# Performance work log

Measured on AMD Instinct MI355X. Metric: run time of the kernel, lower is better.

Reference implementation:

```python
import jax, jax.numpy as jnp
import numpy as np

B, S, F, DK = 4, 2048, 1024, 1024

def setup_inputs() -> dict:
    key = jax.random.key(0)
    ks = jax.random.split(key, 9)
    sF = 1.0 / np.sqrt(F)
    sD = 1.0 / np.sqrt(DK)
    return {
        "x":  jax.random.normal(ks[0], (B, S, F), dtype=jnp.float32),
        "Wq": jax.random.normal(ks[1], (DK, F), dtype=jnp.float32) * sF,
        "bq": jax.random.normal(ks[2], (DK,), dtype=jnp.float32) * sF,
        "Wk": jax.random.normal(ks[3], (DK, F), dtype=jnp.float32) * sF,
        "bk": jax.random.normal(ks[4], (DK,), dtype=jnp.float32) * sF,
        "Wv": jax.random.normal(ks[5], (DK, F), dtype=jnp.float32) * sF,
        "bv": jax.random.normal(ks[6], (DK,), dtype=jnp.float32) * sF,
        "Wo": jax.random.normal(ks[7], (F, DK), dtype=jnp.float32) * sD,
        "bo": jax.random.normal(ks[8], (F,), dtype=jnp.float32) * sD,
    }

def reference(x, Wq, bq, Wk, bk, Wv, bv, Wo, bo):
    # Linear layers (torch convention: y = x @ W.T + b)
    q = jnp.einsum('bsf,df->bsd', x, Wq) + bq  # (B,S,DK)
    k = jnp.einsum('bsf,df->bsd', x, Wk) + bk  # (B,S,DK)
    v = jnp.einsum('bsf,df->bsd', x, Wv) + bv  # (B,S,DK)
    scale = 1.0 / (q.shape[-1] ** 0.5)
    scores = jnp.einsum('bqd,bkd->bqk', q, k) * scale  # (B,Sq,Sk)
    # Faithful to original: softmax over dim=-2 (the QUERY axis)
    attn = jax.nn.softmax(scores, axis=-2)
    ctx = jnp.einsum('bqk,bkd->bqd', attn, v)  # (B,S,DK)
    out = jnp.einsum('bsd,fd->bsf', ctx, Wo) + bo  # (B,S,F)
    return out
```

## Files before the change

### kernel.cpp

```cpp
#include <hip/hip_runtime.h>
#include <hip/hip_bf16.h>
#include <math.h>

typedef __bf16 bf16_t;
typedef __bf16 bf16x8 __attribute__((ext_vector_type(8)));
typedef float f32x4 __attribute__((ext_vector_type(4)));


__device__ __forceinline__ void g2l16(const bf16_t* g, bf16_t* l) {
  __builtin_amdgcn_global_load_lds(
      (const __attribute__((address_space(1))) void*)g,
      (__attribute__((address_space(3))) void*)l, 16, 0, 0);
}

__device__ __forceinline__ float waveSum(float v) {
#pragma unroll
  for (int o = 32; o > 0; o >>= 1) v += __shfl_xor(v, o);
  return v;
}

__device__ __forceinline__ void xcdswz(int& bx, int& by, int& bz) {
  const int gx = gridDim.x, gy = gridDim.y;
  const int n = gx * gy * gridDim.z;
  int f = bx + gx * (by + gy * bz);
  const int cpx = n >> 3;
  int s = (f & 7) * cpx + (f >> 3);
  bx = s % gx; s /= gx; by = s % gy; bz = s / gy;
}

__device__ __forceinline__ bf16x8 rdf(const char* base, int row, int kbyte) {
  int off = (row << 7) + kbyte;
  off ^= (row & 7) << 4;
  return *reinterpret_cast<const bf16x8*>(base + off);
}


__global__ __launch_bounds__(256) void cast_f32_to_bf16(
    const float* __restrict__ in, bf16_t* __restrict__ out, long n) {
  long i = ((long)blockIdx.x * 256 + threadIdx.x) * 8;
  if (i >= n) return;
  float4 a = *reinterpret_cast<const float4*>(in + i);
  float4 b = *reinterpret_cast<const float4*>(in + i + 4);
  bf16x8 o;
  o[0] = (bf16_t)a.x; o[1] = (bf16_t)a.y; o[2] = (bf16_t)a.z; o[3] = (bf16_t)a.w;
  o[4] = (bf16_t)b.x; o[5] = (bf16_t)b.y; o[6] = (bf16_t)b.z; o[7] = (bf16_t)b.w;
  *reinterpret_cast<bf16x8*>(out + i) = o;
}

__global__ __launch_bounds__(256) void cast_w4(
    const float* __restrict__ w0, const float* __restrict__ w1,
    const float* __restrict__ w2, const float* __restrict__ w3,
    bf16_t* __restrict__ o0, bf16_t* __restrict__ o1,
    bf16_t* __restrict__ o2, bf16_t* __restrict__ o3) {
  const int sel = blockIdx.x >> 9;
  const int blk = blockIdx.x & 511;
  const float* in = sel == 0 ? w0 : (sel == 1 ? w1 : (sel == 2 ? w2 : w3));
  bf16_t* out = sel == 0 ? o0 : (sel == 1 ? o1 : (sel == 2 ? o2 : o3));
  long i = ((long)blk * 256 + threadIdx.x) * 8;
  float4 a = *reinterpret_cast<const float4*>(in + i);
  float4 b = *reinterpret_cast<const float4*>(in + i + 4);
  bf16x8 o;
  o[0] = (bf16_t)a.x; o[1] = (bf16_t)a.y; o[2] = (bf16_t)a.z; o[3] = (bf16_t)a.w;
  o[4] = (bf16_t)b.x; o[5] = (bf16_t)b.y; o[6] = (bf16_t)b.z; o[7] = (bf16_t)b.w;
  *reinterpret_cast<bf16x8*>(out + i) = o;
}


#define STAGE256(d, o, h, t) do {                                              \
  const bf16_t* gsrc_ = ((o) ? Bb : Ab) + (long)((h) * 128 + srl) * K +        \
                        (long)(t) * 64 + sgsw;                                 \
  bf16_t* ldsb_ = &lds[d][o][(h) * 8192] + ldst;                               \
  g2l16(gsrc_, ldsb_);                                                         \
  g2l16(gsrc_ + 64L * K, ldsb_ + 4096);                                        \
} while (0)

#define AREAD256(d, qm) do {                                                   \
  const char* Ab_ = (const char*)&lds[d][0][0];                                \
  int r_ = (qm) * 128 + wr2 * 64 + rA;                                         \
  a0 = rdf(Ab_, r_, kb);      a1 = rdf(Ab_, r_, kb + 64);                      \
  a2 = rdf(Ab_, r_ + 16, kb); a3 = rdf(Ab_, r_ + 16, kb + 64);                 \
  a4 = rdf(Ab_, r_ + 32, kb); a5 = rdf(Ab_, r_ + 32, kb + 64);                 \
  a6 = rdf(Ab_, r_ + 48, kb); a7 = rdf(Ab_, r_ + 48, kb + 64);                 \
} while (0)

#define BREAD256(d, qn, r0v, r1v, r2v, r3v) do {                               \
  const char* Bb_ = (const char*)&lds[d][1][0];                                \
  int c_ = (qn) * 128 + wc2 * 32 + rA;                                         \
  r0v = rdf(Bb_, c_, kb);      r1v = rdf(Bb_, c_, kb + 64);                    \
  r2v = rdf(Bb_, c_ + 16, kb); r3v = rdf(Bb_, c_ + 16, kb + 64);               \
} while (0)

#define MFMA16(qm, qn, b0v, b1v, b2v, b3v) do {                                \
  acc[(qm)*4+0][(qn)*2+0] = __builtin_amdgcn_mfma_f32_16x16x32_bf16(a0, b0v, acc[(qm)*4+0][(qn)*2+0], 0,0,0); \
  acc[(qm)*4+0][(qn)*2+0] = __builtin_amdgcn_mfma_f32_16x16x32_bf16(a1, b1v, acc[(qm)*4+0][(qn)*2+0], 0,0,0); \
  acc[(qm)*4+1][(qn)*2+0] = __builtin_amdgcn_mfma_f32_16x16x32_bf16(a2, b0v, acc[(qm)*4+1][(qn)*2+0], 0,0,0); \
  acc[(qm)*4+1][(qn)*2+0] = __builtin_amdgcn_mfma_f32_16x16x32_bf16(a3, b1v, acc[(qm)*4+1][(qn)*2+0], 0,0,0); \
  acc[(qm)*4+2][(qn)*2+0] = __builtin_amdgcn_mfma_f32_16x16x32_bf16(a4, b0v, acc[(qm)*4+2][(qn)*2+0], 0,0,0); \
  acc[(qm)*4+2][(qn)*2+0] = __builtin_amdgcn_mfma_f32_16x16x32_bf16(a5, b1v, acc[(qm)*4+2][(qn)*2+0], 0,0,0); \
  acc[(qm)*4+3][(qn)*2+0] = __builtin_amdgcn_mfma_f32_16x16x32_bf16(a6, b0v, acc[(qm)*4+3][(qn)*2+0], 0,0,0); \
  acc[(qm)*4+3][(qn)*2+0] = __builtin_amdgcn_mfma_f32_16x16x32_bf16(a7, b1v, acc[(qm)*4+3][(qn)*2+0], 0,0,0); \
  acc[(qm)*4+0][(qn)*2+1] = __builtin_amdgcn_mfma_f32_16x16x32_bf16(a0, b2v, acc[(qm)*4+0][(qn)*2+1], 0,0,0); \
  acc[(qm)*4+0][(qn)*2+1] = __builtin_amdgcn_mfma_f32_16x16x32_bf16(a1, b3v, acc[(qm)*4+0][(qn)*2+1], 0,0,0); \
  acc[(qm)*4+1][(qn)*2+1] = __builtin_amdgcn_mfma_f32_16x16x32_bf16(a2, b2v, acc[(qm)*4+1][(qn)*2+1], 0,0,0); \
  acc[(qm)*4+1][(qn)*2+1] = __builtin_amdgcn_mfma_f32_16x16x32_bf16(a3, b3v, acc[(qm)*4+1][(qn)*2+1], 0,0,0); \
  acc[(qm)*4+2][(qn)*2+1] = __builtin_amdgcn_mfma_f32_16x16x32_bf16(a4, b2v, acc[(qm)*4+2][(qn)*2+1], 0,0,0); \
  acc[(qm)*4+2][(qn)*2+1] = __builtin_amdgcn_mfma_f32_16x16x32_bf16(a5, b3v, acc[(qm)*4+2][(qn)*2+1], 0,0,0); \
  acc[(qm)*4+3][(qn)*2+1] = __builtin_amdgcn_mfma_f32_16x16x32_bf16(a6, b2v, acc[(qm)*4+3][(qn)*2+1], 0,0,0); \
  acc[(qm)*4+3][(qn)*2+1] = __builtin_amdgcn_mfma_f32_16x16x32_bf16(a7, b3v, acc[(qm)*4+3][(qn)*2+1], 0,0,0); \
} while (0)

#define VMC(n) asm volatile("s_waitcnt vmcnt(" #n ")" ::: "memory")

#define PH_ENTER() do {                                                        \
  __builtin_amdgcn_s_barrier();                                                \
  asm volatile("s_waitcnt lgkmcnt(0)" ::: "memory");                           \
  __builtin_amdgcn_s_setprio(1);                                               \
} while (0)

#define PH_EXIT() do {                                                         \
  __builtin_amdgcn_s_setprio(0);                                               \
  __builtin_amdgcn_s_barrier();                                                \
} while (0)

template <int EPI>
__launch_bounds__(512, 2)
__global__ void gemm256(const bf16_t* __restrict__ A, const bf16_t* __restrict__ B,
                        int K, float alpha,
                        void* __restrict__ C0, void* __restrict__ C1, void* __restrict__ C2,
                        const float* __restrict__ bias0, const float* __restrict__ bias1,
                        const float* __restrict__ bias2,
                        int Ncols, long sA, long sB, long sC) {
  __shared__ bf16_t lds[2][2][16384];

  int bx = blockIdx.x, by = blockIdx.y, bz = blockIdx.z;
  xcdswz(bx, by, bz);

  const int tid = threadIdx.x;
  const int lane = tid & 63;
  const int w = tid >> 6;
  const int wr2 = w >> 2;
  const int wc2 = w & 3;
  const int rA = lane & 15;
  const int kb = (lane >> 4) << 4;

  const int bm = bx * 256;
  const int bn = by * 256;
  const bf16_t* Ab = A + (long)bz * sA + (long)bm * K;
  const bf16_t* Bb = B + (long)bz * sB + (long)bn * K;

  const int srl = tid >> 3;
  const int sgr = tid & 7;
  const int sgsw = (sgr ^ (srl & 7)) * 8;
  const int ldst = srl * 64 + sgr * 8;

  f32x4 acc[8][4] = {};
  bf16x8 a0, a1, a2, a3, a4, a5, a6, a7;
  bf16x8 p0, p1, p2, p3, q0, q1, q2, q3;

  const int NT = K >> 6;

  STAGE256(0, 0, 0, 0);
  STAGE256(0, 1, 0, 0);
  STAGE256(0, 1, 1, 0);
  STAGE256(0, 0, 1, 0);
  STAGE256(1, 0, 0, 1);
  STAGE256(1, 1, 0, 1);
  STAGE256(1, 1, 1, 1);
  STAGE256(1, 0, 1, 1);
  VMC(12);
  __builtin_amdgcn_s_barrier();

  int t = 0;
  for (int it = 0; it < NT / 2 - 1; ++it, t += 2) {
    AREAD256(0, 0); BREAD256(0, 0, p0, p1, p2, p3);
    VMC(10);
    PH_ENTER(); MFMA16(0, 0, p0, p1, p2, p3); PH_EXIT();
    BREAD256(0, 1, q0, q1, q2, q3);
    STAGE256(0, 0, 0, t + 2); STAGE256(0, 1, 0, t + 2);
    VMC(12);
    PH_ENTER(); MFMA16(0, 1, q0, q1, q2, q3); PH_EXIT();
    AREAD256(0, 1);
    STAGE256(0, 1, 1, t + 2);
    PH_ENTER(); MFMA16(1, 0, p0, p1, p2, p3); PH_EXIT();
    STAGE256(0, 0, 1, t + 2);
    VMC(12);
    PH_ENTER(); MFMA16(1, 1, q0, q1, q2, q3); PH_EXIT();
    AREAD256(1, 0); BREAD256(1, 0, p0, p1, p2, p3);
    VMC(10);
    PH_ENTER(); MFMA16(0, 0, p0, p1, p2, p3); PH_EXIT();
    BREAD256(1, 1, q0, q1, q2, q3);
    STAGE256(1, 0, 0, t + 3); STAGE256(1, 1, 0, t + 3);
    VMC(12);
    PH_ENTER(); MFMA16(0, 1, q0, q1, q2, q3); PH_EXIT();
    AREAD256(1, 1);
    STAGE256(1, 1, 1, t + 3);
    PH_ENTER(); MFMA16(1, 0, p0, p1, p2, p3); PH_EXIT();
    STAGE256(1, 0, 1, t + 3);
    VMC(12);
    PH_ENTER(); MFMA16(1, 1, q0, q1, q2, q3); PH_EXIT();
  }

  AREAD256(0, 0); BREAD256(0, 0, p0, p1, p2, p3);
  VMC(10);
  PH_ENTER(); MFMA16(0, 0, p0, p1, p2, p3); PH_EXIT();
  BREAD256(0, 1, q0, q1, q2, q3);
  VMC(8);
  PH_ENTER(); MFMA16(0, 1, q0, q1, q2, q3); PH_EXIT();
  AREAD256(0, 1);
  PH_ENTER(); MFMA16(1, 0, p0, p1, p2, p3); PH_EXIT();
  VMC(4);
  PH_ENTER(); MFMA16(1, 1, q0, q1, q2, q3); PH_EXIT();
  AREAD256(1, 0); BREAD256(1, 0, p0, p1, p2, p3);
  VMC(2);
  PH_ENTER(); MFMA16(0, 0, p0, p1, p2, p3); PH_EXIT();
  BREAD256(1, 1, q0, q1, q2, q3);
  VMC(0);
  PH_ENTER(); MFMA16(0, 1, q0, q1, q2, q3); PH_EXIT();
  AREAD256(1, 1);
  PH_ENTER(); MFMA16(1, 0, p0, p1, p2, p3); PH_EXIT();
  PH_ENTER(); MFMA16(1, 1, q0, q1, q2, q3); PH_EXIT();

  const int rr = (lane >> 4) * 4;
  const int cc = lane & 15;
#pragma unroll
  for (int qm = 0; qm < 2; ++qm)
#pragma unroll
    for (int m = 0; m < 4; ++m) {
      const int grow = bm + qm * 128 + wr2 * 64 + m * 16 + rr;
#pragma unroll
      for (int qn = 0; qn < 2; ++qn)
#pragma unroll
        for (int n = 0; n < 2; ++n) {
          const int gcol = bn + qn * 128 + wc2 * 32 + n * 16 + cc;
          const f32x4 v = acc[qm * 4 + m][qn * 2 + n];
          if (EPI == 1) {
            const int sel = gcol >> 10;
            const int lcol = gcol & 1023;
            const float* bp = sel == 0 ? bias0 : (sel == 1 ? bias1 : bias2);
            bf16_t* op = sel == 0 ? (bf16_t*)C0 : (sel == 1 ? (bf16_t*)C1 : (bf16_t*)C2);
            const float bv = bp[lcol];
#pragma unroll
            for (int j = 0; j < 4; ++j)
              op[(long)(grow + j) * 1024 + lcol] = (bf16_t)(v[j] + bv);
          } else {
            bf16_t* C = (bf16_t*)C0 + (long)bz * sC;
#pragma unroll
            for (int j = 0; j < 4; ++j)
              C[(long)(grow + j) * Ncols + gcol] = (bf16_t)__expf(v[j] * alpha);
          }
        }
    }
  (void)Ncols;
}


template <int OUT_BF16, int HAS_BIAS>
__launch_bounds__(256, 2)
__global__ void gemm_bt(const bf16_t* __restrict__ A, const bf16_t* __restrict__ B,
                        const float* __restrict__ bias, void* __restrict__ Cv,
                        int M, int N, int K, float alpha,
                        long sA, long sB, long sC) {
  int bxi = blockIdx.x, byi = blockIdx.y, bzi = blockIdx.z;
  xcdswz(bxi, byi, bzi);
  const bf16_t* Ab = A + (long)bzi * sA;
  const bf16_t* Bb = B + (long)bzi * sB;
  const int bm = bxi * 128;
  const int bn = byi * 128;

  __shared__ bf16_t sAt[128 * 32];
  __shared__ bf16_t sBt[128 * 32];

  const int tid = threadIdx.x;
  const int lane = tid & 63;
  const int w = tid >> 6;
  const int wr = (w >> 1) * 64;
  const int wc = (w & 1) * 64;

  f32x4 acc[4][4] = {};

  const int r0 = tid >> 2;
  const int c0 = (tid & 3) * 8;
  const int r1 = 64 + (tid >> 2);
  const long lds0 = (long)tid * 8;
  const long lds1 = 2048 + (long)tid * 8;

  const int arow = wr + (lane & 15);
  const int brow = wc + (lane & 15);
  const int koff = (lane >> 4) * 8;

  const int nK = K >> 5;
  for (int kt = 0; kt < nK; ++kt) {
    const int k0 = kt << 5;
    g2l16(Ab + (long)(bm + r0) * K + k0 + c0, sAt + lds0);
    g2l16(Ab + (long)(bm + r1) * K + k0 + c0, sAt + lds1);
    g2l16(Bb + (long)(bn + r0) * K + k0 + c0, sBt + lds0);
    g2l16(Bb + (long)(bn + r1) * K + k0 + c0, sBt + lds1);
    __syncthreads();

    bf16x8 af[4], bfr[4];
#pragma unroll
    for (int m = 0; m < 4; ++m)
      af[m] = *reinterpret_cast<const bf16x8*>(sAt + (arow + m * 16) * 32 + koff);
#pragma unroll
    for (int n = 0; n < 4; ++n)
      bfr[n] = *reinterpret_cast<const bf16x8*>(sBt + (brow + n * 16) * 32 + koff);
#pragma unroll
    for (int m = 0; m < 4; ++m)
#pragma unroll
      for (int n = 0; n < 4; ++n)
        acc[m][n] = __builtin_amdgcn_mfma_f32_16x16x32_bf16(af[m], bfr[n], acc[m][n], 0, 0, 0);
    __syncthreads();
  }

  const int rbase = bm + wr + (lane >> 4) * 4;
  const int cbase = bn + wc + (lane & 15);
#pragma unroll
  for (int n = 0; n < 4; ++n) {
    const int col = cbase + n * 16;
    float bv = 0.f;
    if (HAS_BIAS) bv = bias[col];
#pragma unroll
    for (int m = 0; m < 4; ++m) {
      const int row0 = rbase + m * 16;
#pragma unroll
      for (int j = 0; j < 4; ++j) {
        float v = acc[m][n][j] * alpha + bv;
        if (OUT_BF16) {
          bf16_t* C = (bf16_t*)Cv + (long)bzi * sC;
          C[(long)(row0 + j) * N + col] = (bf16_t)v;
        } else {
          float* C = (float*)Cv + (long)bzi * sC;
          C[(long)(row0 + j) * N + col] = v;
        }
      }
    }
  }
}


__global__ __launch_bounds__(256) void row_sums(const bf16_t* __restrict__ P,
                                                float* __restrict__ rinv) {
  const long row = blockIdx.x;
  const bf16_t* p = P + row * 2048;
  const int t = threadIdx.x;
  bf16x8 a = *reinterpret_cast<const bf16x8*>(p + t * 8);
  float s = 0.f;
#pragma unroll
  for (int u = 0; u < 8; ++u) s += (float)a[u];
  s = waveSum(s);
  __shared__ float red[4];
  if ((t & 63) == 0) red[t >> 6] = s;
  __syncthreads();
  s = red[0] + red[1] + red[2] + red[3];
  if (t == 0) rinv[row] = 1.0f / s;
}


__global__ __launch_bounds__(256) void scale_T(const bf16_t* __restrict__ P,
                                               const float* __restrict__ rinv,
                                               bf16_t* __restrict__ attn) {
  const int b = blockIdx.z;
  const int q0 = blockIdx.x * 64;
  const int kk0 = blockIdx.y * 64;
  __shared__ bf16_t tile[64][72];
  const int t = threadIdx.x;
  const int i = t >> 2;
  const int qj = (t & 3) * 16;
  const long grow = (long)b * 2048 + kk0 + i;
  const float ri = rinv[grow];
  const bf16_t* src = P + grow * 2048 + q0 + qj;
  bf16x8 v0 = *reinterpret_cast<const bf16x8*>(src);
  bf16x8 v1 = *reinterpret_cast<const bf16x8*>(src + 8);
#pragma unroll
  for (int u = 0; u < 8; ++u) {
    tile[i][qj + u] = (bf16_t)((float)v0[u] * ri);
    tile[i][qj + 8 + u] = (bf16_t)((float)v1[u] * ri);
  }
  __syncthreads();
  const int j = t >> 2;
  const int kc = (t & 3) * 16;
  bf16x8 o0, o1;
#pragma unroll
  for (int u = 0; u < 8; ++u) o0[u] = tile[kc + u][j];
#pragma unroll
  for (int u = 0; u < 8; ++u) o1[u] = tile[kc + 8 + u][j];
  bf16_t* dst = attn + ((long)b * 2048 + q0 + j) * 2048 + kk0 + kc;
  *reinterpret_cast<bf16x8*>(dst) = o0;
  *reinterpret_cast<bf16x8*>(dst + 8) = o1;
}


__global__ __launch_bounds__(256) void transpose_bf16k(const bf16_t* __restrict__ in,
                                                       bf16_t* __restrict__ out,
                                                       int R, int C) {
  const int b = blockIdx.z;
  const int r0 = blockIdx.x * 64;
  const int c0 = blockIdx.y * 64;
  __shared__ bf16_t tile[64][72];
  const int t = threadIdx.x;
  const int i = t >> 2;
  const int cj = (t & 3) * 16;
  const bf16_t* src = in + ((long)b * R + r0 + i) * C + c0 + cj;
  bf16x8 a0 = *reinterpret_cast<const bf16x8*>(src);
  bf16x8 a1 = *reinterpret_cast<const bf16x8*>(src + 8);
#pragma unroll
  for (int u = 0; u < 8; ++u) { tile[i][cj + u] = a0[u]; tile[i][cj + 8 + u] = a1[u]; }
  __syncthreads();
  const int j = t >> 2;
  const int rc = (t & 3) * 16;
  bf16x8 o0, o1;
#pragma unroll
  for (int u = 0; u < 8; ++u) o0[u] = tile[rc + u][j];
#pragma unroll
  for (int u = 0; u < 8; ++u) o1[u] = tile[rc + 8 + u][j];
  bf16_t* dst = out + ((long)b * C + c0 + j) * R + r0 + rc;
  *reinterpret_cast<bf16x8*>(dst) = o0;
  *reinterpret_cast<bf16x8*>(dst + 8) = o1;
}


extern "C" void kernel_launch(void* const* d_in, const int* in_sizes, int n_in,
                              void* d_out, int out_size, void* d_ws, size_t ws_size,
                              hipStream_t stream) {
  const float* x  = (const float*)d_in[0];
  const float* Wq = (const float*)d_in[1];
  const float* bq = (const float*)d_in[2];
  const float* Wk = (const float*)d_in[3];
  const float* bk = (const float*)d_in[4];
  const float* Wv = (const float*)d_in[5];
  const float* bv = (const float*)d_in[6];
  const float* Wo = (const float*)d_in[7];
  const float* bo = (const float*)d_in[8];
  float* out = (float*)d_out;
  char* ws = (char*)d_ws;

  const long MB = 1024L * 1024L;
  bf16_t* xb    = (bf16_t*)(ws + 0);
  bf16_t* Wqkvb = (bf16_t*)(ws + 16 * MB);
  bf16_t* Wob   = (bf16_t*)(ws + 22 * MB);
  bf16_t* Qb    = (bf16_t*)(ws + 24 * MB);
  bf16_t* Kb    = (bf16_t*)(ws + 40 * MB);
  bf16_t* Vb    = (bf16_t*)(ws + 56 * MB);
  bf16_t* Pp    = (bf16_t*)(ws + 72 * MB);
  bf16_t* attn  = (bf16_t*)(ws + 136 * MB);
  float*  rinv  = (float*)(ws + 168 * MB);
  bf16_t* VT    = (bf16_t*)(ws + 0);
  bf16_t* ctxb  = (bf16_t*)(ws + 24 * MB);

  cast_f32_to_bf16<<<4096, 256, 0, stream>>>(x, xb, 8388608);
  cast_w4<<<2048, 256, 0, stream>>>(Wq, Wk, Wv, Wo,
                                    Wqkvb, Wqkvb + 1048576, Wqkvb + 2097152, Wob);

  gemm256<1><<<dim3(32, 12, 1), 512, 0, stream>>>(
      xb, Wqkvb, 1024, 1.0f, Qb, Kb, Vb, bq, bk, bv, 3072, 0, 0, 0);

  gemm256<2><<<dim3(8, 8, 4), 512, 0, stream>>>(
      Kb, Qb, 1024, 0.03125f, Pp, nullptr, nullptr, nullptr, nullptr, nullptr,
      2048, 2048L * 1024, 2048L * 1024, 2048L * 2048);

  row_sums<<<8192, 256, 0, stream>>>(Pp, rinv);
  dim3 gsm(32, 32, 4);
  scale_T<<<gsm, 256, 0, stream>>>(Pp, rinv, attn);

  dim3 gtr(32, 16, 4);
  transpose_bf16k<<<gtr, 256, 0, stream>>>(Vb, VT, 2048, 1024);

  dim3 gctx(16, 8, 4);
  gemm_bt<1, 0><<<gctx, 256, 0, stream>>>(attn, VT, nullptr, ctxb, 2048, 1024, 2048, 1.0f,
                                          2048L * 2048, 1024L * 2048, 2048L * 1024);

  dim3 gout(64, 8, 1);
  gemm_bt<0, 1><<<gout, 256, 0, stream>>>(ctxb, Wob, bo, out, 8192, 1024, 1024, 1.0f, 0, 0, 0);

  (void)in_sizes; (void)n_in; (void)out_size; (void)ws_size;
}
```

Baseline: 314.4 us.

## Fold softmax column normalization into V and use 256-tile GEMM for output projection

```diff
diff --git a/kernel.cpp b/kernel.cpp
--- a/kernel.cpp
+++ b/kernel.cpp
@@ -11,12 +11,6 @@
   __builtin_amdgcn_global_load_lds(
       (const __attribute__((address_space(1))) void*)g,
       (__attribute__((address_space(3))) void*)l, 16, 0, 0);
-}
-
-__device__ __forceinline__ float waveSum(float v) {
-#pragma unroll
-  for (int o = 32; o > 0; o >>= 1) v += __shfl_xor(v, o);
-  return v;
 }
 
 __device__ __forceinline__ void xcdswz(int& bx, int& by, int& bz) {
@@ -242,11 +236,17 @@
 #pragma unroll
             for (int j = 0; j < 4; ++j)
               op[(long)(grow + j) * 1024 + lcol] = (bf16_t)(v[j] + bv);
-          } else {
+          } else if (EPI == 2) {
             bf16_t* C = (bf16_t*)C0 + (long)bz * sC;
 #pragma unroll
             for (int j = 0; j < 4; ++j)
               C[(long)(grow + j) * Ncols + gcol] = (bf16_t)__expf(v[j] * alpha);
+          } else {
+            float* C = (float*)C0;
+            const float bv = bias0[gcol];
+#pragma unroll
+            for (int j = 0; j < 4; ++j)
+              C[(long)(grow + j) * Ncols + gcol] = v[j] + bv;
           }
         }
     }
@@ -338,61 +338,33 @@
 }
 
 
-__global__ __launch_bounds__(256) void row_sums(const bf16_t* __restrict__ P,
-                                                float* __restrict__ rinv) {
-  const long row = blockIdx.x;
-  const bf16_t* p = P + row * 2048;
+__global__ __launch_bounds__(256) void col_partial(const bf16_t* __restrict__ P,
+                                                   float* __restrict__ part) {
+  const int kc = blockIdx.x, qc = blockIdx.y, b = blockIdx.z;
   const int t = threadIdx.x;
-  bf16x8 a = *reinterpret_cast<const bf16x8*>(p + t * 8);
-  float s = 0.f;
-#pragma unroll
-  for (int u = 0; u < 8; ++u) s += (float)a[u];
-  s = waveSum(s);
-  __shared__ float red[4];
-  if ((t & 63) == 0) red[t >> 6] = s;
+  const int tk = t & 31;
+  const int tq = t >> 5;
+  const bf16_t* base = P + ((long)b * 2048 + (long)qc * 256 + tq) * 2048 + kc * 256 + tk * 8;
+  float s[8] = {};
+  for (int q = 0; q < 256; q += 8) {
+    bf16x8 v = *reinterpret_cast<const bf16x8*>(base + (long)q * 2048);
+#pragma unroll
+    for (int u = 0; u < 8; ++u) s[u] += (float)v[u];
+  }
+  __shared__ float red[8][256];
+#pragma unroll
+  for (int u = 0; u < 8; ++u) red[tq][tk * 8 + u] = s[u];
   __syncthreads();
-  s = red[0] + red[1] + red[2] + red[3];
-  if (t == 0) rinv[row] = 1.0f / s;
-}
-
-
-__global__ __launch_bounds__(256) void scale_T(const bf16_t* __restrict__ P,
-                                               const float* __restrict__ rinv,
-                                               bf16_t* __restrict__ attn) {
-  const int b = blockIdx.z;
-  const int q0 = blockIdx.x * 64;
-  const int kk0 = blockIdx.y * 64;
-  __shared__ bf16_t tile[64][72];
-  const int t = threadIdx.x;
-  const int i = t >> 2;
-  const int qj = (t & 3) * 16;
-  const long grow = (long)b * 2048 + kk0 + i;
-  const float ri = rinv[grow];
-  const bf16_t* src = P + grow * 2048 + q0 + qj;
-  bf16x8 v0 = *reinterpret_cast<const bf16x8*>(src);
-  bf16x8 v1 = *reinterpret_cast<const bf16x8*>(src + 8);
-#pragma unroll
-  for (int u = 0; u < 8; ++u) {
-    tile[i][qj + u] = (bf16_t)((float)v0[u] * ri);
-    tile[i][qj + 8 + u] = (bf16_t)((float)v1[u] * ri);
-  }
-  __syncthreads();
-  const int j = t >> 2;
-  const int kc = (t & 3) * 16;
-  bf16x8 o0, o1;
-#pragma unroll
-  for (int u = 0; u < 8; ++u) o0[u] = tile[kc + u][j];
-#pragma unroll
-  for (int u = 0; u < 8; ++u) o1[u] = tile[kc + 8 + u][j];
-  bf16_t* dst = attn + ((long)b * 2048 + q0 + j) * 2048 + kk0 + kc;
-  *reinterpret_cast<bf16x8*>(dst) = o0;
-  *reinterpret_cast<bf16x8*>(dst + 8) = o1;
-}
-
-
-__global__ __launch_bounds__(256) void transpose_bf16k(const bf16_t* __restrict__ in,
-                                                       bf16_t* __restrict__ out,
-                                                       int R, int C) {
+  float tot = 0.f;
+#pragma unroll
+  for (int r = 0; r < 8; ++r) tot += red[r][t];
+  part[((long)b * 8 + qc) * 2048 + kc * 256 + t] = tot;
+}
+
+
+__global__ __launch_bounds__(256) void vscale_T(const bf16_t* __restrict__ V,
+                                                const float* __restrict__ part,
+                                                bf16_t* __restrict__ VsT) {
   const int b = blockIdx.z;
   const int r0 = blockIdx.x * 64;
   const int c0 = blockIdx.y * 64;
@@ -400,11 +372,19 @@
   const int t = threadIdx.x;
   const int i = t >> 2;
   const int cj = (t & 3) * 16;
-  const bf16_t* src = in + ((long)b * R + r0 + i) * C + c0 + cj;
+  const int k = r0 + i;
+  float rs = 0.f;
+#pragma unroll
+  for (int r = 0; r < 8; ++r) rs += part[((long)b * 8 + r) * 2048 + k];
+  const float ri = 1.0f / rs;
+  const bf16_t* src = V + ((long)b * 2048 + k) * 1024 + c0 + cj;
   bf16x8 a0 = *reinterpret_cast<const bf16x8*>(src);
   bf16x8 a1 = *reinterpret_cast<const bf16x8*>(src + 8);
 #pragma unroll
-  for (int u = 0; u < 8; ++u) { tile[i][cj + u] = a0[u]; tile[i][cj + 8 + u] = a1[u]; }
+  for (int u = 0; u < 8; ++u) {
+    tile[i][cj + u] = (bf16_t)((float)a0[u] * ri);
+    tile[i][cj + 8 + u] = (bf16_t)((float)a1[u] * ri);
+  }
   __syncthreads();
   const int j = t >> 2;
   const int rc = (t & 3) * 16;
@@ -413,7 +393,7 @@
   for (int u = 0; u < 8; ++u) o0[u] = tile[rc + u][j];
 #pragma unroll
   for (int u = 0; u < 8; ++u) o1[u] = tile[rc + 8 + u][j];
-  bf16_t* dst = out + ((long)b * C + c0 + j) * R + r0 + rc;
+  bf16_t* dst = VsT + ((long)b * 1024 + c0 + j) * 2048 + r0 + rc;
   *reinterpret_cast<bf16x8*>(dst) = o0;
   *reinterpret_cast<bf16x8*>(dst + 8) = o1;
 }
@@ -442,9 +422,8 @@
   bf16_t* Kb    = (bf16_t*)(ws + 40 * MB);
   bf16_t* Vb    = (bf16_t*)(ws + 56 * MB);
   bf16_t* Pp    = (bf16_t*)(ws + 72 * MB);
-  bf16_t* attn  = (bf16_t*)(ws + 136 * MB);
-  float*  rinv  = (float*)(ws + 168 * MB);
-  bf16_t* VT    = (bf16_t*)(ws + 0);
+  float*  part  = (float*)(ws + 168 * MB);
+  bf16_t* VsT   = (bf16_t*)(ws + 0);
   bf16_t* ctxb  = (bf16_t*)(ws + 24 * MB);
 
   cast_f32_to_bf16<<<4096, 256, 0, stream>>>(x, xb, 8388608);
@@ -455,22 +434,20 @@
       xb, Wqkvb, 1024, 1.0f, Qb, Kb, Vb, bq, bk, bv, 3072, 0, 0, 0);
 
   gemm256<2><<<dim3(8, 8, 4), 512, 0, stream>>>(
-      Kb, Qb, 1024, 0.03125f, Pp, nullptr, nullptr, nullptr, nullptr, nullptr,
+      Qb, Kb, 1024, 0.03125f, Pp, nullptr, nullptr, nullptr, nullptr, nullptr,
       2048, 2048L * 1024, 2048L * 1024, 2048L * 2048);
 
-  row_sums<<<8192, 256, 0, stream>>>(Pp, rinv);
-  dim3 gsm(32, 32, 4);
-  scale_T<<<gsm, 256, 0, stream>>>(Pp, rinv, attn);
-
-  dim3 gtr(32, 16, 4);
-  transpose_bf16k<<<gtr, 256, 0, stream>>>(Vb, VT, 2048, 1024);
+  col_partial<<<dim3(8, 8, 4), 256, 0, stream>>>(Pp, part);
+
+  vscale_T<<<dim3(32, 16, 4), 256, 0, stream>>>(Vb, part, VsT);
 
   dim3 gctx(16, 8, 4);
-  gemm_bt<1, 0><<<gctx, 256, 0, stream>>>(attn, VT, nullptr, ctxb, 2048, 1024, 2048, 1.0f,
+  gemm_bt<1, 0><<<gctx, 256, 0, stream>>>(Pp, VsT, nullptr, ctxb, 2048, 1024, 2048, 1.0f,
                                           2048L * 2048, 1024L * 2048, 2048L * 1024);
 
-  dim3 gout(64, 8, 1);
-  gemm_bt<0, 1><<<gout, 256, 0, stream>>>(ctxb, Wob, bo, out, 8192, 1024, 1024, 1.0f, 0, 0, 0);
+  gemm256<3><<<dim3(32, 4, 1), 512, 0, stream>>>(
+      ctxb, Wob, 1024, 1.0f, out, nullptr, nullptr, bo, nullptr, nullptr,
+      1024, 0, 0, 0);
 
   (void)in_sizes; (void)n_in; (void)out_size; (void)ws_size;
 }
```

Measured after the change: 300.1 us. -4.5%, faster.
